# Performance work log

Measured on AMD Instinct MI355X. Metric: run time of the kernel, lower is better.

## Reference

```python
import jax, jax.numpy as jnp
import numpy as np

N_NODES = 16384   # total nodes
B = 32            # graphs in batch
NPG = 512         # nodes per graph (uniform -> dense mask is all True)
E = 262144        # edges (avg degree 16)
H = 64            # hidden_dim
HEADS = 8
DH = H // HEADS


def setup_inputs() -> dict:
    key = jax.random.key(0)
    ks = jax.random.split(key, 20)
    x = jax.random.normal(ks[0], (N_NODES, H), dtype=jnp.float32)
    # edges constrained within each graph of 512 nodes
    src = jax.random.randint(ks[1], (E,), 0, N_NODES, dtype=jnp.int32)
    dst = (src // NPG) * NPG + jax.random.randint(ks[2], (E,), 0, NPG, dtype=jnp.int32)
    edge_index = jnp.stack([src, dst])
    batch = (jnp.arange(N_NODES, dtype=jnp.int32) // NPG)
    c_size = jnp.full((B,), NPG, dtype=jnp.int32)
    s = 1.0 / np.sqrt(H)
    p = lambda k, shape: (jax.random.normal(k, shape, dtype=jnp.float32) * s)
    return {
        "x": x,
        "w_gat": p(ks[3], (H, H)), "att_src": p(ks[4], (H,)), "att_dst": p(ks[5], (H,)), "b_gat": jnp.zeros((H,), jnp.float32),
        "g1": jnp.ones((H,), jnp.float32), "b1": jnp.zeros((H,), jnp.float32),
        "wq": p(ks[6], (H, H)), "bq": jnp.zeros((H,), jnp.float32),
        "wk": p(ks[7], (H, H)), "bk": jnp.zeros((H,), jnp.float32),
        "wv": p(ks[8], (H, H)), "bv": jnp.zeros((H,), jnp.float32),
        "wo": p(ks[9], (H, H)), "bo": jnp.zeros((H,), jnp.float32),
        "g2": jnp.ones((H,), jnp.float32), "b2": jnp.zeros((H,), jnp.float32),
        "edge_index": edge_index, "batch": batch, "c_size": c_size,
    }


def _layer_norm(x, g, b):
    mu = jnp.mean(x, axis=-1, keepdims=True)
    var = jnp.var(x, axis=-1, keepdims=True)
    return (x - mu) * jax.lax.rsqrt(var + 1e-5) * g + b


def _gat_conv(x, edge_index, w, a_src, a_dst, bias):
    # PyG GATConv, 1 head, add_self_loops=True, leaky_relu slope 0.2
    n = x.shape[0]
    loops = jnp.arange(n, dtype=edge_index.dtype)
    src = jnp.concatenate([edge_index[0], loops])
    dst = jnp.concatenate([edge_index[1], loops])
    h = x @ w                                  # [n, H]
    e = jax.nn.leaky_relu((h @ a_src)[src] + (h @ a_dst)[dst], 0.2)  # [E+n]
    m = jax.ops.segment_max(e, dst, num_segments=n)
    p = jnp.exp(e - m[dst])
    s = jax.ops.segment_sum(p, dst, num_segments=n)
    alpha = p / (s[dst] + 1e-16)
    out = jax.ops.segment_sum(alpha[:, None] * h[src], dst, num_segments=n)
    return out + bias


def reference(x, w_gat, att_src, att_dst, b_gat, g1, b1,
              wq, bq, wk, bk, wv, bv, wo, bo, g2, b2,
              edge_index, batch, c_size):
    # GAT branch (dropout is identity in eval)
    x_ = jax.nn.relu(_gat_conv(x, edge_index, w_gat, att_src, att_dst, b_gat))
    x1 = _layer_norm(x + x_, g1, b1)                     # [n, H]
    # to_dense_batch: uniform graphs -> mask all True, plain reshape
    xd = x1.reshape(B, NPG, H)
    q = (xd @ wq + bq).reshape(B, NPG, HEADS, DH)
    k = (xd @ wk + bk).reshape(B, NPG, HEADS, DH)
    v = (xd @ wv + bv).reshape(B, NPG, HEADS, DH)
    scores = jnp.einsum('bqhd,bkhd->bhqk', q, k) / np.sqrt(DH)  # [B,h,N,N]
    attn = jax.nn.softmax(scores, axis=-1)
    o = jnp.einsum('bhqk,bkhd->bqhd', attn, v).reshape(B, NPG, H)
    o = o @ wo + bo
    x2 = _layer_norm(x1 + jax.nn.relu(o.reshape(N_NODES, H)), g2, b2)
    return x2  # recon_loss is None in eval mode
```

## Files before the change

### kernel.cpp

```cpp
#include <hip/hip_runtime.h>
#include <hip/hip_bf16.h>
#include <hip/hip_fp16.h>

#define NN     16384
#define HD     64
#define BG     32
#define NPG    512
#define NHEADS 8
#define DH     8
#define DEGMAX 40

#define QS_STR 12
#define KS_STR 12
#define VT_STR 264

typedef __hip_bfloat16 bf16;
typedef _Float16 v4h __attribute__((ext_vector_type(4)));
typedef float v16f __attribute__((ext_vector_type(16)));

#if defined(__has_builtin)
#if __has_builtin(__builtin_amdgcn_exp2f)
#define EXP2F(x) __builtin_amdgcn_exp2f(x)
#else
#define EXP2F(x) exp2f(x)
#endif
#if __has_builtin(__builtin_amdgcn_fdot2)
#define HAS_FDOT2 1
#endif
#else
#define EXP2F(x) exp2f(x)
#endif

#ifdef HAS_FDOT2
typedef _Float16 hvec2 __attribute__((ext_vector_type(2)));
#endif

__device__ __forceinline__ float fdot2u(unsigned a, unsigned b, float c) {
#ifdef HAS_FDOT2
  union { unsigned u; hvec2 v; } x, y;
  x.u = a; y.u = b;
  return __builtin_amdgcn_fdot2(x.v, y.v, c, false);
#else
  union { unsigned u; __half2 h; } x, y;
  x.u = a; y.u = b;
  return fmaf(__low2float(x.h), __low2float(y.h),
              fmaf(__high2float(x.h), __high2float(y.h), c));
#endif
}

__device__ __forceinline__ float b2f(bf16 v) { return __bfloat162float(v); }

__device__ __forceinline__ float ldf(const void* p, int i, int bf) {
  return bf ? __bfloat162float(((const bf16*)p)[i]) : ((const float*)p)[i];
}

__device__ __forceinline__ float wave_sum(float v) {
#pragma unroll
  for (int off = 32; off > 0; off >>= 1) v += __shfl_xor(v, off);
  return v;
}

__device__ __forceinline__ unsigned packh2(float a, float b) {
  union { unsigned u; __half2 h; } z;
  z.h = __floats2half2_rn(a, b);
  return z.u;
}

__device__ __forceinline__ int detect_bf(const unsigned short* xr, int tid, int nt) {
  __shared__ int s_cnt;
  if (tid == 0) s_cnt = 0;
  __syncthreads();
  int sane = 0;
  for (int i = tid; i < 256; i += nt) {
    int e = (xr[2 * i] >> 7) & 0xFF;
    sane += (e >= 100 && e <= 150) ? 1 : 0;
  }
  if (sane) atomicAdd(&s_cnt, sane);
  __syncthreads();
  return s_cnt > 180;
}

__global__ __launch_bounds__(256) void k_prep(
    const void* __restrict__ x, const void* __restrict__ w,
    const void* __restrict__ wo,
    int* __restrict__ cur, uint2* __restrict__ wgp, uint2* __restrict__ wop,
    int* __restrict__ flagp)
{
  const int tid = threadIdx.x, b = blockIdx.x;
  if (b < 64) {
    cur[b * 256 + tid] = 0;
    return;
  }
  const int bf = detect_bf((const unsigned short*)x, tid, 256);
  if (b == 64 && tid == 0) *flagp = bf;
  const void* src = (b == 64) ? w : wo;
  uint2* dst = (b == 64) ? wgp : wop;
  for (int e = tid; e < 1024; e += 256) {
    const int ln = e & 31, ct = (e >> 5) & 1, hh = (e >> 6) & 1, kt = e >> 7;
    const int kr = kt * 8 + 4 * hh, col = ct * 32 + ln;
    uint2 v;
    v.x = packh2(ldf(src, (kr + 0) * HD + col, bf),
                 ldf(src, (kr + 1) * HD + col, bf));
    v.y = packh2(ldf(src, (kr + 2) * HD + col, bf),
                 ldf(src, (kr + 3) * HD + col, bf));
    dst[e] = v;
  }
}

__global__ __launch_bounds__(64) void k_build(
    const void* __restrict__ x, const uint2* __restrict__ wgp,
    const void* __restrict__ asrc, const void* __restrict__ adst,
    const int* __restrict__ esrc, const int* __restrict__ edst, int E,
    int* __restrict__ cur, int* __restrict__ ell,
    bf16* __restrict__ h, float* __restrict__ as_, float* __restrict__ ad_,
    const int* __restrict__ dflag)
{
  const int t = threadIdx.x;
  const int ln = t & 31, hh = t >> 5;
  const int bf = *dflag;
  for (int e = blockIdx.x * 64 + t; e < E; e += gridDim.x * 64) {
    int d = edst[e];
    int k = atomicAdd(&cur[d], 1);
    if (k < DEGMAX) ell[d * DEGMAX + k] = esrc[e];
  }
  const int base = blockIdx.x * 32;
  v16f c0, c1;
#pragma unroll
  for (int i = 0; i < 16; ++i) { c0[i] = 0.f; c1[i] = 0.f; }
#pragma unroll
  for (int kt = 0; kt < 8; ++kt) {
    const int kr = kt * 8 + 4 * hh;
    union { unsigned u[2]; v4h v; } A, B0, B1;
    if (bf) {
      uint2 xv = *(const uint2*)((const unsigned short*)x +
                                 (size_t)(base + ln) * HD + kr);
      A.u[0] = packh2(__uint_as_float(xv.x << 16),
                      __uint_as_float(xv.x & 0xffff0000u));
      A.u[1] = packh2(__uint_as_float(xv.y << 16),
                      __uint_as_float(xv.y & 0xffff0000u));
    } else {
      float4 xv = *(const float4*)((const float*)x +
                                   (size_t)(base + ln) * HD + kr);
      A.u[0] = packh2(xv.x, xv.y);
      A.u[1] = packh2(xv.z, xv.w);
    }
    uint2 b0 = wgp[((kt * 2 + hh) * 2 + 0) * 32 + ln];
    uint2 b1 = wgp[((kt * 2 + hh) * 2 + 1) * 32 + ln];
    B0.u[0] = b0.x; B0.u[1] = b0.y;
    B1.u[0] = b1.x; B1.u[1] = b1.y;
    c0 = __builtin_amdgcn_mfma_f32_32x32x8f16(A.v, B0.v, c0, 0, 0, 0);
    c1 = __builtin_amdgcn_mfma_f32_32x32x8f16(A.v, B1.v, c1, 0, 0, 0);
  }
  const float av0 = ldf(asrc, ln, bf), av1 = ldf(asrc, 32 + ln, bf);
  const float dv0 = ldf(adst, ln, bf), dv1 = ldf(adst, 32 + ln, bf);
#pragma unroll
  for (int r = 0; r < 16; ++r) {
    const int node = base + (r & 3) + 8 * (r >> 2) + 4 * hh;
    h[node * HD + ln]      = __float2bfloat16(c0[r]);
    h[node * HD + 32 + ln] = __float2bfloat16(c1[r]);
    float pa = c0[r] * av0 + c1[r] * av1;
    float pd = c0[r] * dv0 + c1[r] * dv1;
#pragma unroll
    for (int off = 16; off > 0; off >>= 1) {
      pa += __shfl_xor(pa, off);
      pd += __shfl_xor(pd, off);
    }
    if (ln == 0) { as_[node] = pa; ad_[node] = pd; }
  }
}

__global__ __launch_bounds__(256) void k_gather(
    const void* __restrict__ x, const int* __restrict__ cur,
    const int* __restrict__ ell, const float* __restrict__ as_,
    const float* __restrict__ ad_, const bf16* __restrict__ h,
    const void* __restrict__ bg, const void* __restrict__ g1,
    const void* __restrict__ b1,
    const void* __restrict__ wq, const void* __restrict__ bq,
    const void* __restrict__ wk, const void* __restrict__ bk,
    const void* __restrict__ wv, const void* __restrict__ bv,
    const int* __restrict__ dflag,
    unsigned* __restrict__ wpk, float* __restrict__ bpk,
    __half* __restrict__ x1)
{
  const int tid = threadIdx.x, lane = tid & 63, wid = tid >> 6;
  const int bf = *dflag;
  if (blockIdx.x < 4) {
    for (int idx = blockIdx.x * 256 + tid; idx < 3 * 32 * 64; idx += 1024) {
      int m = idx >> 11;
      int r = idx & 2047;
      int kp = r >> 6, col = r & 63;
      const void* ws = (m == 0) ? wq : (m == 1) ? wk : wv;
      wpk[idx] = packh2(ldf(ws, (2 * kp) * HD + col, bf),
                        ldf(ws, (2 * kp + 1) * HD + col, bf));
    }
  } else if (blockIdx.x == 4 && tid < 192) {
    int m = tid >> 6, col = tid & 63;
    const void* bs = (m == 0) ? bq : (m == 1) ? bk : bv;
    bpk[tid] = ldf(bs, col, bf);
  }
  const int n = blockIdx.x * 4 + wid;
  const float adn = ad_[n];
  float e0 = as_[n] + adn;
  e0 = e0 > 0.f ? e0 : 0.2f * e0;
  float den = __expf(fminf(e0, 30.f));
  float num = den * b2f(h[n * HD + lane]);
  const int deg = min(cur[n], DEGMAX);
  const int* row = ell + n * DEGMAX;
  int i = 0;
  for (; i + 8 <= deg; i += 8) {
    int s[8];
#pragma unroll
    for (int k = 0; k < 8; ++k) s[k] = row[i + k];
    float a[8], hh[8];
#pragma unroll
    for (int k = 0; k < 8; ++k) a[k] = as_[s[k]];
#pragma unroll
    for (int k = 0; k < 8; ++k) hh[k] = b2f(h[s[k] * HD + lane]);
#pragma unroll
    for (int k = 0; k < 8; ++k) {
      float e = a[k] + adn;
      e = e > 0.f ? e : 0.2f * e;
      float p = __expf(fminf(e, 30.f));
      den += p;
      num = fmaf(p, hh[k], num);
    }
  }
  for (; i + 4 <= deg; i += 4) {
    int s0 = row[i], s1 = row[i + 1], s2 = row[i + 2], s3 = row[i + 3];
    float a0 = as_[s0], a1 = as_[s1], a2 = as_[s2], a3 = as_[s3];
    float h0 = b2f(h[s0 * HD + lane]), h1 = b2f(h[s1 * HD + lane]);
    float h2 = b2f(h[s2 * HD + lane]), h3 = b2f(h[s3 * HD + lane]);
    float e_0 = a0 + adn; e_0 = e_0 > 0.f ? e_0 : 0.2f * e_0;
    float e_1 = a1 + adn; e_1 = e_1 > 0.f ? e_1 : 0.2f * e_1;
    float e_2 = a2 + adn; e_2 = e_2 > 0.f ? e_2 : 0.2f * e_2;
    float e_3 = a3 + adn; e_3 = e_3 > 0.f ? e_3 : 0.2f * e_3;
    float p0 = __expf(fminf(e_0, 30.f)), p1 = __expf(fminf(e_1, 30.f));
    float p2 = __expf(fminf(e_2, 30.f)), p3 = __expf(fminf(e_3, 30.f));
    den += p0 + p1 + p2 + p3;
    num = fmaf(p0, h0, num); num = fmaf(p1, h1, num);
    num = fmaf(p2, h2, num); num = fmaf(p3, h3, num);
  }
  for (; i < deg; ++i) {
    int s = row[i];
    float e = as_[s] + adn;
    e = e > 0.f ? e : 0.2f * e;
    float p = __expf(fminf(e, 30.f));
    den += p;
    num = fmaf(p, b2f(h[s * HD + lane]), num);
  }
  float v = num / (den + 1e-16f) + ldf(bg, lane, bf);
  v = fmaxf(v, 0.f) + ldf(x, n * HD + lane, bf);
  float mu = wave_sum(v) * (1.f / 64.f);
  float dv = v - mu;
  float var = wave_sum(dv * dv) * (1.f / 64.f);
  float r = rsqrtf(var + 1e-5f);
  x1[n * HD + lane] =
      __float2half(dv * r * ldf(g1, lane, bf) + ldf(b1, lane, bf));
}

__global__ __launch_bounds__(512, 2) void k_attn13(
    const __half* __restrict__ x1,
    const unsigned* __restrict__ wpk, const float* __restrict__ bpk,
    bf16* __restrict__ num_t, float* __restrict__ den_t)
{
  const int t = threadIdx.x;
  __shared__ _Float16 Qs[NPG * QS_STR];
  __shared__ _Float16 Ks[256 * KS_STR];
  __shared__ _Float16 Vt[DH * VT_STR];
  const int bid = blockIdx.x;
  const int g = bid >> 4, hd = (bid >> 1) & 7, half = bid & 1;
  const float qscale = 0.3535533905932738f * 1.4426950408889634f;
  {
    const int r = t & 255;
    const int m = (t < 256) ? 1 : 2;
    const uint4* xk4 = (const uint4*)(x1 + (size_t)(g * NPG + half * 256 + r) * HD);
    const unsigned* wb0 = wpk + m * 2048 + hd * 8;
    float acc[DH];
#pragma unroll
    for (int j = 0; j < DH; ++j) acc[j] = bpk[m * 64 + hd * 8 + j];
#pragma unroll
    for (int blk = 0; blk < 8; ++blk) {
      uint4 xp = xk4[blk];
      const unsigned* wb = wb0 + blk * 256;
#pragma unroll
      for (int j = 0; j < DH; ++j) {
        acc[j] = fdot2u(xp.x, wb[j], acc[j]);
        acc[j] = fdot2u(xp.y, wb[64 + j], acc[j]);
        acc[j] = fdot2u(xp.z, wb[128 + j], acc[j]);
        acc[j] = fdot2u(xp.w, wb[192 + j], acc[j]);
      }
    }
    if (t < 256) {
      unsigned w0 = packh2(acc[0], acc[1]), w1 = packh2(acc[2], acc[3]);
      unsigned w2 = packh2(acc[4], acc[5]), w3 = packh2(acc[6], acc[7]);
      *(uint2*)(Ks + r * KS_STR) = make_uint2(w0, w1);
      *(uint2*)(Ks + r * KS_STR + 4) = make_uint2(w2, w3);
    } else {
#pragma unroll
      for (int j = 0; j < DH; ++j) Vt[j * VT_STR + r] = (_Float16)acc[j];
    }
  }
  {
    const uint4* xa4 = (const uint4*)(x1 + (size_t)(g * NPG + t) * HD);
    const unsigned* wb0 = wpk + hd * 8;
    float qa[DH];
#pragma unroll
    for (int j = 0; j < DH; ++j) qa[j] = bpk[hd * 8 + j];
#pragma unroll
    for (int blk = 0; blk < 8; ++blk) {
      uint4 xp = xa4[blk];
      const unsigned* wb = wb0 + blk * 256;
#pragma unroll
      for (int j = 0; j < DH; ++j) {
        qa[j] = fdot2u(xp.x, wb[j], qa[j]);
        qa[j] = fdot2u(xp.y, wb[64 + j], qa[j]);
        qa[j] = fdot2u(xp.z, wb[128 + j], qa[j]);
        qa[j] = fdot2u(xp.w, wb[192 + j], qa[j]);
      }
    }
    unsigned w0 = packh2(qa[0] * qscale, qa[1] * qscale);
    unsigned w1 = packh2(qa[2] * qscale, qa[3] * qscale);
    unsigned w2 = packh2(qa[4] * qscale, qa[5] * qscale);
    unsigned w3 = packh2(qa[6] * qscale, qa[7] * qscale);
    *(uint2*)(Qs + t * QS_STR) = make_uint2(w0, w1);
    *(uint2*)(Qs + t * QS_STR + 4) = make_uint2(w2, w3);
  }
  __syncthreads();
  const int lane = t & 63, wid = t >> 6;
  const int ln = lane & 31, hh = lane >> 5;
  const int plane = half * 8 + hd;
  const size_t obase = (size_t)plane * NN + (size_t)g * NPG;
  v16f zf;
#pragma unroll
  for (int i = 0; i < 16; ++i) zf[i] = 0.f;
#pragma unroll
  for (int qt = 0; qt < 2; ++qt) {
    const int qbase = (wid * 2 + qt) * 32;
    v4h qf = *(const v4h*)(Qs + (qbase + ln) * QS_STR + 4 * hh);
    v16f oacc = zf;
    float den = 0.f;
#pragma unroll
    for (int kt = 0; kt < 8; ++kt) {
      v4h kf = *(const v4h*)(Ks + (kt * 32 + ln) * KS_STR + 4 * hh);
      v16f s = __builtin_amdgcn_mfma_f32_32x32x8f16(kf, qf, zf, 0, 0, 0);
#pragma unroll
      for (int g2 = 0; g2 < 4; ++g2) {
        float e0 = EXP2F(s[4 * g2 + 0]);
        float e1 = EXP2F(s[4 * g2 + 1]);
        float e2 = EXP2F(s[4 * g2 + 2]);
        float e3 = EXP2F(s[4 * g2 + 3]);
        den += (e0 + e1) + (e2 + e3);
        union { unsigned u[2]; v4h v; } pu;
        pu.u[0] = packh2(e0, e1);
        pu.u[1] = packh2(e2, e3);
        v4h vf = *(const v4h*)(Vt + (ln & 7) * VT_STR + kt * 32 + g2 * 8 + 4 * hh);
        oacc = __builtin_amdgcn_mfma_f32_32x32x8f16(pu.v, vf, oacc, 0, 0, 0);
      }
    }
    den += __shfl_xor(den, 32);
    if (lane < 32) den_t[obase + qbase + lane] = den;
#pragma unroll
    for (int r = 0; r < 16; ++r) {
      const int q = qbase + (r & 3) + 8 * (r >> 2) + 4 * hh;
      if (ln < 8)
        num_t[(obase + q) * 8 + ln] = __float2bfloat16(oacc[r]);
    }
  }
}

__global__ __launch_bounds__(64) void k_out(
    const bf16* __restrict__ num_t, const float* __restrict__ den_t,
    const __half* __restrict__ x1, const uint2* __restrict__ wop,
    const void* __restrict__ bo,
    const void* __restrict__ g2, const void* __restrict__ b2,
    const int* __restrict__ dflag, void* __restrict__ out)
{
  const int t = threadIdx.x;
  const int bf = *dflag;
  const int ln = t & 31, hh = t >> 5;
  const int base = blockIdx.x * 32;
  const int n = base + ln;
  v16f c0, c1;
#pragma unroll
  for (int i = 0; i < 16; ++i) { c0[i] = 0.f; c1[i] = 0.f; }
#pragma unroll
  for (int kt = 0; kt < 8; ++kt) {
    union { uint2 u; unsigned short s[4]; } L, H;
    L.u = *(const uint2*)(num_t + ((size_t)kt * NN + n) * 8 + 4 * hh);
    H.u = *(const uint2*)(num_t + ((size_t)(8 + kt) * NN + n) * 8 + 4 * hh);
    float den = den_t[(size_t)kt * NN + n] + den_t[(size_t)(8 + kt) * NN + n];
    float rden = 1.f / den;
    float o0 = (__uint_as_float((unsigned)L.s[0] << 16) +
                __uint_as_float((unsigned)H.s[0] << 16)) * rden;
    float o1 = (__uint_as_float((unsigned)L.s[1] << 16) +
                __uint_as_float((unsigned)H.s[1] << 16)) * rden;
    float o2 = (__uint_as_float((unsigned)L.s[2] << 16) +
                __uint_as_float((unsigned)H.s[2] << 16)) * rden;
    float o3 = (__uint_as_float((unsigned)L.s[3] << 16) +
                __uint_as_float((unsigned)H.s[3] << 16)) * rden;
    union { unsigned u[2]; v4h v; } A, B0, B1;
    A.u[0] = packh2(o0, o1);
    A.u[1] = packh2(o2, o3);
    uint2 b0 = wop[((kt * 2 + hh) * 2 + 0) * 32 + ln];
    uint2 b1 = wop[((kt * 2 + hh) * 2 + 1) * 32 + ln];
    B0.u[0] = b0.x; B0.u[1] = b0.y;
    B1.u[0] = b1.x; B1.u[1] = b1.y;
    c0 = __builtin_amdgcn_mfma_f32_32x32x8f16(A.v, B0.v, c0, 0, 0, 0);
    c1 = __builtin_amdgcn_mfma_f32_32x32x8f16(A.v, B1.v, c1, 0, 0, 0);
  }
  const float bo0 = ldf(bo, ln, bf),      bo1 = ldf(bo, 32 + ln, bf);
  const float g20 = ldf(g2, ln, bf),      g21 = ldf(g2, 32 + ln, bf);
  const float b20 = ldf(b2, ln, bf),      b21 = ldf(b2, 32 + ln, bf);
#pragma unroll
  for (int r = 0; r < 16; ++r) {
    const int node = base + (r & 3) + 8 * (r >> 2) + 4 * hh;
    float t0 = __half2float(x1[node * HD + ln]) + fmaxf(c0[r] + bo0, 0.f);
    float t1 = __half2float(x1[node * HD + 32 + ln]) + fmaxf(c1[r] + bo1, 0.f);
    float s = t0 + t1;
#pragma unroll
    for (int off = 1; off < 32; off <<= 1) s += __shfl_xor(s, off);
    const float mu = s * (1.f / 64.f);
    const float d0 = t0 - mu, d1 = t1 - mu;
    float v = d0 * d0 + d1 * d1;
#pragma unroll
    for (int off = 1; off < 32; off <<= 1) v += __shfl_xor(v, off);
    const float rr = rsqrtf(v * (1.f / 64.f) + 1e-5f);
    const float r0 = d0 * rr * g20 + b20;
    const float r1 = d1 * rr * g21 + b21;
    if (bf) {
      ((bf16*)out)[node * HD + ln]      = __float2bfloat16(r0);
      ((bf16*)out)[node * HD + 32 + ln] = __float2bfloat16(r1);
    } else {
      ((float*)out)[node * HD + ln]      = r0;
      ((float*)out)[node * HD + 32 + ln] = r1;
    }
  }
}

extern "C" void kernel_launch(void* const* d_in, const int* in_sizes, int n_in,
                              void* d_out, int out_size, void* d_ws, size_t ws_size,
                              hipStream_t stream)
{
  const void* x    = d_in[0];
  const void* wgat = d_in[1];
  const void* asrc = d_in[2];
  const void* adst = d_in[3];
  const void* bgat = d_in[4];
  const void* g1   = d_in[5];
  const void* b1   = d_in[6];
  const void* wq   = d_in[7];
  const void* bq   = d_in[8];
  const void* wk   = d_in[9];
  const void* bk   = d_in[10];
  const void* wv   = d_in[11];
  const void* bv   = d_in[12];
  const void* wo   = d_in[13];
  const void* bo   = d_in[14];
  const void* g2   = d_in[15];
  const void* b2   = d_in[16];
  const int*  ei   = (const int*)d_in[17];
  const int E = in_sizes[17] / 2;
  const int* esrc = ei;
  const int* edst = ei + E;

  char* W = (char*)d_ws;
  __half* x1b  = (__half*)W;
  int*   ell   = (int*)(W + (size_t)(2 << 20));
  bf16*  hb    = (bf16*)(W + (size_t)(2 << 20) + (size_t)NN * DEGMAX * 4);
  bf16*  num_t = (bf16*)(W + (size_t)(2 << 20));
  float* den_t = (float*)(W + (size_t)(6 << 20));
  float* as_   = (float*)(W + (size_t)(7 << 20));
  float* ad_   = as_ + NN;
  int*   cur   = (int*)(ad_ + NN);
  int*   flag  = cur + NN;
  unsigned* wpk = (unsigned*)(flag + 1);
  float* bpk   = (float*)(wpk + 3 * 32 * 64);
  uint2* wgp   = (uint2*)(bpk + 192);
  uint2* wop   = wgp + 1024;

  k_prep   <<<66, 256, 0, stream>>>(x, wgat, wo, cur, wgp, wop, flag);
  k_build  <<<NN / 32, 64, 0, stream>>>(x, wgp, asrc, adst, esrc, edst, E,
                                        cur, ell, hb, as_, ad_, flag);
  k_gather <<<NN / 4, 256, 0, stream>>>(x, cur, ell, as_, ad_, hb,
                                        bgat, g1, b1,
                                        wq, bq, wk, bk, wv, bv,
                                        flag, wpk, bpk, x1b);
  k_attn13 <<<BG * NHEADS * 2, 512, 0, stream>>>(x1b, wpk, bpk, num_t, den_t);
  k_out    <<<NN / 32, 64, 0, stream>>>(num_t, den_t, x1b, wop, bo, g2, b2,
                                        flag, d_out);
}
```

Baseline: 171.6 us.

## Process full key range per attention block instead of splitting keys in halves

The attention kernel now uses one 1024-thread block per (graph, head) that projects K and V for all 512 keys, instead of two 512-thread blocks that each handle half the keys. This removes the duplicated Q projection across the two key halves, and the output kernel no longer has to read and merge two partial numerator/denominator planes. Q projection is split across thread pairs and combined with a lane shuffle. The cost is half as many blocks (256), bigger blocks with more LDS each, and a longer serial key loop per wave, which can lower occupancy and latency hiding.

```diff
diff --git a/kernel.cpp b/kernel.cpp
--- a/kernel.cpp
+++ b/kernel.cpp
@@ -12,7 +12,7 @@
 
 #define QS_STR 12
 #define KS_STR 12
-#define VT_STR 264
+#define VT_STR 520
 
 typedef __hip_bfloat16 bf16;
 typedef _Float16 v4h __attribute__((ext_vector_type(4)));
@@ -258,22 +258,22 @@
       __float2half(dv * r * ldf(g1, lane, bf) + ldf(b1, lane, bf));
 }
 
-__global__ __launch_bounds__(512, 2) void k_attn13(
+__global__ __launch_bounds__(1024) void k_attn13(
     const __half* __restrict__ x1,
     const unsigned* __restrict__ wpk, const float* __restrict__ bpk,
     bf16* __restrict__ num_t, float* __restrict__ den_t)
 {
   const int t = threadIdx.x;
   __shared__ _Float16 Qs[NPG * QS_STR];
-  __shared__ _Float16 Ks[256 * KS_STR];
+  __shared__ _Float16 Ks[NPG * KS_STR];
   __shared__ _Float16 Vt[DH * VT_STR];
   const int bid = blockIdx.x;
-  const int g = bid >> 4, hd = (bid >> 1) & 7, half = bid & 1;
+  const int g = bid >> 3, hd = bid & 7;
   const float qscale = 0.3535533905932738f * 1.4426950408889634f;
   {
-    const int r = t & 255;
-    const int m = (t < 256) ? 1 : 2;
-    const uint4* xk4 = (const uint4*)(x1 + (size_t)(g * NPG + half * 256 + r) * HD);
+    const int r = t & 511;
+    const int m = (t < 512) ? 1 : 2;
+    const uint4* xk4 = (const uint4*)(x1 + (size_t)(g * NPG + r) * HD);
     const unsigned* wb0 = wpk + m * 2048 + hd * 8;
     float acc[DH];
 #pragma unroll
@@ -290,7 +290,7 @@
         acc[j] = fdot2u(xp.w, wb[192 + j], acc[j]);
       }
     }
-    if (t < 256) {
+    if (t < 512) {
       unsigned w0 = packh2(acc[0], acc[1]), w1 = packh2(acc[2], acc[3]);
       unsigned w2 = packh2(acc[4], acc[5]), w3 = packh2(acc[6], acc[7]);
       *(uint2*)(Ks + r * KS_STR) = make_uint2(w0, w1);
@@ -301,13 +301,15 @@
     }
   }
   {
-    const uint4* xa4 = (const uint4*)(x1 + (size_t)(g * NPG + t) * HD);
+    const int qr = t >> 1, lo = t & 1;
+    const uint4* xa4 = (const uint4*)(x1 + (size_t)(g * NPG + qr) * HD);
     const unsigned* wb0 = wpk + hd * 8;
     float qa[DH];
 #pragma unroll
-    for (int j = 0; j < DH; ++j) qa[j] = bpk[hd * 8 + j];
-#pragma unroll
-    for (int blk = 0; blk < 8; ++blk) {
+    for (int j = 0; j < DH; ++j) qa[j] = lo ? 0.f : bpk[hd * 8 + j];
+#pragma unroll
+    for (int b = 0; b < 4; ++b) {
+      const int blk = lo * 4 + b;
       uint4 xp = xa4[blk];
       const unsigned* wb = wb0 + blk * 256;
 #pragma unroll
@@ -318,53 +320,53 @@
         qa[j] = fdot2u(xp.w, wb[192 + j], qa[j]);
       }
     }
-    unsigned w0 = packh2(qa[0] * qscale, qa[1] * qscale);
-    unsigned w1 = packh2(qa[2] * qscale, qa[3] * qscale);
-    unsigned w2 = packh2(qa[4] * qscale, qa[5] * qscale);
-    unsigned w3 = packh2(qa[6] * qscale, qa[7] * qscale);
-    *(uint2*)(Qs + t * QS_STR) = make_uint2(w0, w1);
-    *(uint2*)(Qs + t * QS_STR + 4) = make_uint2(w2, w3);
+#pragma unroll
+    for (int j = 0; j < DH; ++j) qa[j] += __shfl_xor(qa[j], 1);
+    if (!lo) {
+      unsigned w0 = packh2(qa[0] * qscale, qa[1] * qscale);
+      unsigned w1 = packh2(qa[2] * qscale, qa[3] * qscale);
+      unsigned w2 = packh2(qa[4] * qscale, qa[5] * qscale);
+      unsigned w3 = packh2(qa[6] * qscale, qa[7] * qscale);
+      *(uint2*)(Qs + qr * QS_STR) = make_uint2(w0, w1);
+      *(uint2*)(Qs + qr * QS_STR + 4) = make_uint2(w2, w3);
+    }
   }
   __syncthreads();
   const int lane = t & 63, wid = t >> 6;
   const int ln = lane & 31, hh = lane >> 5;
-  const int plane = half * 8 + hd;
-  const size_t obase = (size_t)plane * NN + (size_t)g * NPG;
+  const size_t obase = (size_t)hd * NN + (size_t)g * NPG;
   v16f zf;
 #pragma unroll
   for (int i = 0; i < 16; ++i) zf[i] = 0.f;
-#pragma unroll
-  for (int qt = 0; qt < 2; ++qt) {
-    const int qbase = (wid * 2 + qt) * 32;
-    v4h qf = *(const v4h*)(Qs + (qbase + ln) * QS_STR + 4 * hh);
-    v16f oacc = zf;
-    float den = 0.f;
-#pragma unroll
-    for (int kt = 0; kt < 8; ++kt) {
-      v4h kf = *(const v4h*)(Ks + (kt * 32 + ln) * KS_STR + 4 * hh);
-      v16f s = __builtin_amdgcn_mfma_f32_32x32x8f16(kf, qf, zf, 0, 0, 0);
-#pragma unroll
-      for (int g2 = 0; g2 < 4; ++g2) {
-        float e0 = EXP2F(s[4 * g2 + 0]);
-        float e1 = EXP2F(s[4 * g2 + 1]);
-        float e2 = EXP2F(s[4 * g2 + 2]);
-        float e3 = EXP2F(s[4 * g2 + 3]);
-        den += (e0 + e1) + (e2 + e3);
-        union { unsigned u[2]; v4h v; } pu;
-        pu.u[0] = packh2(e0, e1);
-        pu.u[1] = packh2(e2, e3);
-        v4h vf = *(const v4h*)(Vt + (ln & 7) * VT_STR + kt * 32 + g2 * 8 + 4 * hh);
-        oacc = __builtin_amdgcn_mfma_f32_32x32x8f16(pu.v, vf, oacc, 0, 0, 0);
-      }
-    }
-    den += __shfl_xor(den, 32);
-    if (lane < 32) den_t[obase + qbase + lane] = den;
-#pragma unroll
-    for (int r = 0; r < 16; ++r) {
-      const int q = qbase + (r & 3) + 8 * (r >> 2) + 4 * hh;
-      if (ln < 8)
-        num_t[(obase + q) * 8 + ln] = __float2bfloat16(oacc[r]);
-    }
+  const int qbase = wid * 32;
+  v4h qf = *(const v4h*)(Qs + (qbase + ln) * QS_STR + 4 * hh);
+  v16f oacc = zf;
+  float den = 0.f;
+#pragma unroll
+  for (int kt = 0; kt < 16; ++kt) {
+    v4h kf = *(const v4h*)(Ks + (kt * 32 + ln) * KS_STR + 4 * hh);
+    v16f s = __builtin_amdgcn_mfma_f32_32x32x8f16(kf, qf, zf, 0, 0, 0);
+#pragma unroll
+    for (int g2 = 0; g2 < 4; ++g2) {
+      float e0 = EXP2F(s[4 * g2 + 0]);
+      float e1 = EXP2F(s[4 * g2 + 1]);
+      float e2 = EXP2F(s[4 * g2 + 2]);
+      float e3 = EXP2F(s[4 * g2 + 3]);
+      den += (e0 + e1) + (e2 + e3);
+      union { unsigned u[2]; v4h v; } pu;
+      pu.u[0] = packh2(e0, e1);
+      pu.u[1] = packh2(e2, e3);
+      v4h vf = *(const v4h*)(Vt + (ln & 7) * VT_STR + kt * 32 + g2 * 8 + 4 * hh);
+      oacc = __builtin_amdgcn_mfma_f32_32x32x8f16(pu.v, vf, oacc, 0, 0, 0);
+    }
+  }
+  den += __shfl_xor(den, 32);
+  if (lane < 32) den_t[obase + qbase + lane] = den;
+#pragma unroll
+  for (int r = 0; r < 16; ++r) {
+    const int q = qbase + (r & 3) + 8 * (r >> 2) + 4 * hh;
+    if (ln < 8)
+      num_t[(obase + q) * 8 + ln] = __float2bfloat16(oacc[r]);
   }
 }
 
@@ -385,19 +387,13 @@
   for (int i = 0; i < 16; ++i) { c0[i] = 0.f; c1[i] = 0.f; }
 #pragma unroll
   for (int kt = 0; kt < 8; ++kt) {
-    union { uint2 u; unsigned short s[4]; } L, H;
+    union { uint2 u; unsigned short s[4]; } L;
     L.u = *(const uint2*)(num_t + ((size_t)kt * NN + n) * 8 + 4 * hh);
-    H.u = *(const uint2*)(num_t + ((size_t)(8 + kt) * NN + n) * 8 + 4 * hh);
-    float den = den_t[(size_t)kt * NN + n] + den_t[(size_t)(8 + kt) * NN + n];
-    float rden = 1.f / den;
-    float o0 = (__uint_as_float((unsigned)L.s[0] << 16) +
-                __uint_as_float((unsigned)H.s[0] << 16)) * rden;
-    float o1 = (__uint_as_float((unsigned)L.s[1] << 16) +
-                __uint_as_float((unsigned)H.s[1] << 16)) * rden;
-    float o2 = (__uint_as_float((unsigned)L.s[2] << 16) +
-                __uint_as_float((unsigned)H.s[2] << 16)) * rden;
-    float o3 = (__uint_as_float((unsigned)L.s[3] << 16) +
-                __uint_as_float((unsigned)H.s[3] << 16)) * rden;
+    float rden = 1.f / den_t[(size_t)kt * NN + n];
+    float o0 = __uint_as_float((unsigned)L.s[0] << 16) * rden;
+    float o1 = __uint_as_float((unsigned)L.s[1] << 16) * rden;
+    float o2 = __uint_as_float((unsigned)L.s[2] << 16) * rden;
+    float o3 = __uint_as_float((unsigned)L.s[3] << 16) * rden;
     union { unsigned u[2]; v4h v; } A, B0, B1;
     A.u[0] = packh2(o0, o1);
     A.u[1] = packh2(o2, o3);
@@ -485,7 +481,7 @@
                                         bgat, g1, b1,
                                         wq, bq, wk, bk, wv, bv,
                                         flag, wpk, bpk, x1b);
-  k_attn13 <<<BG * NHEADS * 2, 512, 0, stream>>>(x1b, wpk, bpk, num_t, den_t);
+  k_attn13 <<<BG * NHEADS, 1024, 0, stream>>>(x1b, wpk, bpk, num_t, den_t);
   k_out    <<<NN / 32, 64, 0, stream>>>(num_t, den_t, x1b, wop, bo, g2, b2,
                                         flag, d_out);
 }
```

New measurement: 175.4 us. +2.3%, slower.
